# Kernel tuning notes

Measured on AMD Instinct MI355X. Metric: run time of the kernel, lower is better.

Reference implementation:

```python
import jax, jax.numpy as jnp
import numpy as np

B, S, HID = 1, 2048, 2048
NH, NKV, D = 32, 4, 128   # query heads, kv heads, head_dim
ROPE_THETA = 1e6
EPS = 1e-6


def _rms_norm(x, w):
    # per-head RMSNorm over head_dim, computed in fp32 (Qwen3MoeRMSNorm)
    xf = x.astype(jnp.float32)
    var = jnp.mean(xf * xf, axis=-1, keepdims=True)
    return (w * (xf * jax.lax.rsqrt(var + EPS))).astype(x.dtype)


def _rotate_half(x):
    x1, x2 = jnp.split(x, 2, axis=-1)
    return jnp.concatenate([-x2, x1], axis=-1)


def setup_inputs() -> dict:
    key = jax.random.key(0)
    ks = jax.random.split(key, 5)
    hidden_states = jax.random.normal(ks[0], (B, S, HID), jnp.float32)
    # weights stored as (in, out); torch Linear computes x @ W.T with W (out,in) -- same math
    wq = jax.random.normal(ks[1], (HID, NH * D), jnp.float32) * 0.02
    wk = jax.random.normal(ks[2], (HID, NKV * D), jnp.float32) * 0.02
    wv = jax.random.normal(ks[3], (HID, NKV * D), jnp.float32) * 0.02
    wo = jax.random.normal(ks[4], (NH * D, HID), jnp.float32) * 0.02
    q_norm_w = jnp.ones((D,), jnp.float32)
    k_norm_w = jnp.ones((D,), jnp.float32)
    # RoPE tables (rotate_half convention, like HF Qwen3)
    inv_freq = 1.0 / (ROPE_THETA ** (jnp.arange(0, D, 2, dtype=jnp.float32) / D))
    freqs = jnp.arange(S, dtype=jnp.float32)[:, None] * inv_freq[None, :]  # [S, D/2]
    emb = jnp.concatenate([freqs, freqs], axis=-1)  # [S, D]
    cos, sin = jnp.cos(emb), jnp.sin(emb)
    # causal mask (True = keep)
    attention_mask = jnp.tril(jnp.ones((S, S), bool))[None, None]
    return {
        'hidden_states': hidden_states, 'cos': cos, 'sin': sin,
        'wq': wq, 'wk': wk, 'wv': wv, 'wo': wo,
        'q_norm_w': q_norm_w, 'k_norm_w': k_norm_w,
        'attention_mask': attention_mask, 'start_pos': 0,
    }


def reference(hidden_states, cos, sin, wq, wk, wv, wo, q_norm_w, k_norm_w,
              attention_mask, start_pos):
    b, s, _ = hidden_states.shape
    # projections + per-head RMSNorm, then [B, H, S, D]
    q = _rms_norm((hidden_states @ wq).reshape(b, s, NH, D), q_norm_w).transpose(0, 2, 1, 3)
    k = _rms_norm((hidden_states @ wk).reshape(b, s, NKV, D), k_norm_w).transpose(0, 2, 1, 3)
    v = (hidden_states @ wv).reshape(b, s, NKV, D).transpose(0, 2, 1, 3)
    # rotary embedding (rotate_half form); start_pos=0 -> tables already aligned
    c = cos[None, None, :, :]
    sn = sin[None, None, :, :]
    q = q * c + _rotate_half(q) * sn
    k = k * c + _rotate_half(k) * sn
    # GQA: repeat kv heads to match query heads
    groups = NH // NKV
    k = jnp.repeat(k, groups, axis=1)
    v = jnp.repeat(v, groups, axis=1)
    scaling = D ** -0.5
    scores = jnp.einsum('bhqd,bhkd->bhqk', q, k) * scaling  # [B, NH, S, S]
    scores = jnp.where(attention_mask, scores, jnp.float32(-1e9))
    attn = jax.nn.softmax(scores, axis=-1)
    out = jnp.einsum('bhqk,bhkd->bhqd', attn, v)  # [B, NH, S, D]
    out = out.transpose(0, 2, 1, 3).reshape(b, s, NH * D)
    return out @ wo
```

## Files before the change

### kernel.cpp

```cpp
#include <hip/hip_runtime.h>
#include <hip/hip_bf16.h>

using short4v = __attribute__((ext_vector_type(4))) short;
using short8 = __attribute__((ext_vector_type(8))) short;
using f32x4  = __attribute__((ext_vector_type(4))) float;

#define SEQ 2048
#define NHEAD 32
#define NKVH 4
#define HDIM 128
#define QK_SCALE_LOG2 (0.08838834764831845f * 1.44269504088896340f)

__device__ __forceinline__ float fast_exp2(float x) { return __builtin_amdgcn_exp2f(x); }
__device__ __forceinline__ float b2f(short u) {
    return __uint_as_float(((unsigned)(unsigned short)u) << 16);
}
__device__ __forceinline__ short f2bb(float f) {
    __hip_bfloat16 h = __float2bfloat16(f);
    return *reinterpret_cast<short*>(&h);
}
__device__ __forceinline__ void gload_lds16(const __hip_bfloat16* src, __hip_bfloat16* dst) {
    __builtin_amdgcn_global_load_lds((const __attribute__((address_space(1))) void*)src,
                                     (__attribute__((address_space(3))) void*)dst, 16, 0, 0);
}

__global__ __launch_bounds__(256) void prep_kernel(
    const float* __restrict__ hs, __hip_bfloat16* __restrict__ hsb,
    const float* __restrict__ wq, const float* __restrict__ wk, const float* __restrict__ wv,
    const float* __restrict__ wo,
    __hip_bfloat16* __restrict__ WqkvT, __hip_bfloat16* __restrict__ WoT) {
    const int b = blockIdx.x, tid = threadIdx.x;
    if (b < 4096) {
        int i = b * 256 + tid;
        float4 v = ((const float4*)hs)[i];
        __hip_bfloat16 h4[4] = {__float2bfloat16(v.x), __float2bfloat16(v.y),
                                __float2bfloat16(v.z), __float2bfloat16(v.w)};
        ((ushort4*)hsb)[i] = *(ushort4*)h4;
        return;
    }
    __shared__ float tile[32][33];
    const float* W; __hip_bfloat16* Wt; int N, ld, nb, kb;
    if (b < 12288)      { int bb = b - 4096;  W = wq; Wt = WqkvT;                       N = 4096; ld = 2048; nb = (bb & 127) * 32; kb = (bb >> 7) * 32; }
    else if (b < 13312) { int bb = b - 12288; W = wk; Wt = WqkvT + (size_t)4096 * 2048; N = 512;  ld = 2048; nb = (bb & 15) * 32;  kb = (bb >> 4) * 32; }
    else if (b < 14336) { int bb = b - 13312; W = wv; Wt = WqkvT + (size_t)4608 * 2048; N = 512;  ld = 2048; nb = (bb & 15) * 32;  kb = (bb >> 4) * 32; }
    else                { int bb = b - 14336; W = wo; Wt = WoT;                         N = 2048; ld = 4096; nb = (bb & 63) * 32;  kb = (bb >> 6) * 32; }
    int tx = tid & 31, ty = tid >> 5;
    for (int j = 0; j < 32; j += 8)
        tile[ty + j][tx] = W[(size_t)(kb + ty + j) * N + nb + tx];
    __syncthreads();
    for (int j = 0; j < 32; j += 8)
        Wt[(size_t)(nb + ty + j) * ld + kb + tx] = __float2bfloat16(tile[tx][ty + j]);
}

__global__ void add3b_kernel(const __hip_bfloat16* __restrict__ a, const __hip_bfloat16* __restrict__ b,
                             const __hip_bfloat16* __restrict__ c, float* __restrict__ o, int n4) {
    int i = blockIdx.x * blockDim.x + threadIdx.x;
    if (i >= n4) return;
    short4v x = ((const short4v*)a)[i];
    short4v y = ((const short4v*)b)[i];
    short4v z = ((const short4v*)c)[i];
    float4 r = {b2f(x[0]) + b2f(y[0]) + b2f(z[0]), b2f(x[1]) + b2f(y[1]) + b2f(z[1]),
                b2f(x[2]) + b2f(y[2]) + b2f(z[2]), b2f(x[3]) + b2f(y[3]) + b2f(z[3])};
    ((float4*)o)[i] = r;
}

#define BM 128
#define BN 128
#define BK2 64
template <typename OutT>
__global__ __launch_bounds__(256) void gemm_bt_kernel(
    const __hip_bfloat16* __restrict__ A, const __hip_bfloat16* __restrict__ Bt,
    OutT* __restrict__ C, int M, int N, int KextMax, int ld, int koff, long long czstride, int Ktot) {
    const int kstart = blockIdx.z * koff;
    const int Kext = min(KextMax, Ktot - kstart);
    A  += (size_t)kstart;
    Bt += (size_t)kstart;
    C  += (size_t)blockIdx.z * czstride;
    __shared__ __align__(16) __hip_bfloat16 sA[BM * BK2];
    __shared__ __align__(16) __hip_bfloat16 sB[BN * BK2];
    const int tid = threadIdx.x;
    const int w = tid >> 6, l = tid & 63;
    const int wr = w >> 1, wc = w & 1;
    const int row0 = blockIdx.y * BM;
    const int col0 = blockIdx.x * BN;
    const int fr = l & 15;
    const int fq = l >> 4;
    const int xs = (fr & 7) << 4;

    f32x4 acc[4][4] = {};

    for (int k0 = 0; k0 < Kext; k0 += BK2) {
        for (int i = 0; i < 4; ++i) {
            int ch = i * 256 + tid;
            int row = ch >> 3;
            int cb = ((ch & 7) * 16) ^ ((row & 7) << 4);
            gload_lds16(A  + (size_t)(row0 + row) * ld + k0 + (cb >> 1), &sA[ch * 8]);
            gload_lds16(Bt + (size_t)(col0 + row) * ld + k0 + (cb >> 1), &sB[ch * 8]);
        }
        __syncthreads();
        short8 af[4][2], bfr[4][2];
        for (int m = 0; m < 4; ++m) {
            const char* base = (const char*)sA + (wr * 64 + m * 16 + fr) * 128;
            af[m][0] = *(const short8*)(base + (((fq) * 16)     ^ xs));
            af[m][1] = *(const short8*)(base + (((fq + 4) * 16) ^ xs));
        }
        for (int n = 0; n < 4; ++n) {
            const char* base = (const char*)sB + (wc * 64 + n * 16 + fr) * 128;
            bfr[n][0] = *(const short8*)(base + (((fq) * 16)     ^ xs));
            bfr[n][1] = *(const short8*)(base + (((fq + 4) * 16) ^ xs));
        }
        for (int kk = 0; kk < 2; ++kk)
            for (int m = 0; m < 4; ++m)
                for (int n = 0; n < 4; ++n)
                    acc[m][n] = __builtin_amdgcn_mfma_f32_16x16x32_bf16(af[m][kk], bfr[n][kk], acc[m][n], 0, 0, 0);
        __syncthreads();
    }
    for (int m = 0; m < 4; ++m)
        for (int n = 0; n < 4; ++n)
            for (int r = 0; r < 4; ++r) {
                int row = row0 + wr * 64 + m * 16 + fq * 4 + r;
                int col = col0 + wc * 64 + n * 16 + fr;
                float v = acc[m][n][r];
                if constexpr (__is_same(OutT, float)) C[(size_t)row * N + col] = v;
                else C[(size_t)row * N + col] = __float2bfloat16(v);
            }
}

__global__ __launch_bounds__(256) void pack_kernel(
    const __hip_bfloat16* __restrict__ P0, const __hip_bfloat16* __restrict__ P1,
    const float* __restrict__ cosp, const float* __restrict__ sinp,
    const float* __restrict__ qnw, const float* __restrict__ knw,
    __hip_bfloat16* __restrict__ Qh, __hip_bfloat16* __restrict__ Kh, __hip_bfloat16* __restrict__ Vt) {
    const int tid = threadIdx.x;
    const int rloc = tid >> 4, l16 = tid & 15;
    const int r = blockIdx.y * 16 + rloc;
    const int s = blockIdx.x * 2 + (r >= 40 ? 1 : 0);
    const int slot = (r >= 40) ? r - 40 : r;
    int off;
    if (slot < 32)      off = slot * 128;
    else if (slot < 36) off = 4096 + (slot - 32) * 128;
    else                off = 4608 + (slot - 36) * 128;
    const int d0 = l16 * 4;
    const size_t base = (size_t)s * 5120 + off;

    short4v a0 = *(const short4v*)&P0[base + d0];
    short4v a1 = *(const short4v*)&P0[base + d0 + 64];
    short4v b0 = *(const short4v*)&P1[base + d0];
    short4v b1 = *(const short4v*)&P1[base + d0 + 64];
    float x1[4], x2[4];
    for (int j = 0; j < 4; ++j) {
        x1[j] = b2f(a0[j]) + b2f(b0[j]);
        x2[j] = b2f(a1[j]) + b2f(b1[j]);
    }

    if (slot >= 36) {
        int t = slot - 36;
        for (int j = 0; j < 4; ++j) {
            Vt[((size_t)t * 128 + d0 + j) * SEQ + s]      = __float2bfloat16(x1[j]);
            Vt[((size_t)t * 128 + d0 + 64 + j) * SEQ + s] = __float2bfloat16(x2[j]);
        }
        return;
    }
    float ss = 0.f;
    for (int j = 0; j < 4; ++j) ss += x1[j] * x1[j] + x2[j] * x2[j];
    for (int x = 1; x < 16; x <<= 1) ss += __shfl_xor(ss, x);
    float rs = rsqrtf(ss * (1.0f / 128.0f) + 1e-6f);

    f32x4 c4 = *(const f32x4*)&cosp[(size_t)s * 128 + d0];
    f32x4 s4 = *(const f32x4*)&sinp[(size_t)s * 128 + d0];
    const float* wgt = (slot < 32) ? qnw : knw;
    f32x4 w1 = *(const f32x4*)&wgt[d0];
    f32x4 w2 = *(const f32x4*)&wgt[d0 + 64];
    const float scl = (slot < 32) ? QK_SCALE_LOG2 : 1.0f;

    short4v o1, o2;
    for (int j = 0; j < 4; ++j) {
        float a = x1[j] * rs * w1[j], b = x2[j] * rs * w2[j];
        o1[j] = f2bb((a * c4[j] - b * s4[j]) * scl);
        o2[j] = f2bb((b * c4[j] + a * s4[j]) * scl);
    }
    __hip_bfloat16* dst;
    if (slot < 32) dst = Qh + ((size_t)slot * SEQ + s) * 128;
    else           dst = Kh + ((size_t)(slot - 32) * SEQ + s) * 128;
    *(short4v*)&dst[d0]      = o1;
    *(short4v*)&dst[d0 + 64] = o2;
}

__global__ __launch_bounds__(256, 2) void attn_kernel(
    const __hip_bfloat16* __restrict__ Qh,
    const __hip_bfloat16* __restrict__ Kh,
    const __hip_bfloat16* __restrict__ Vt,
    __hip_bfloat16* __restrict__ Oa) {
    __shared__ __align__(16) __hip_bfloat16 sK[2][64 * 128];
    __shared__ __align__(16) __hip_bfloat16 sV[2][128 * 64];
    __shared__ __align__(16) __hip_bfloat16 sP[4][16 * 72];

    const int tid = threadIdx.x;
    const int w = tid >> 6, l = tid & 63;
    const int bx = blockIdx.x;
    const int y = bx & 7;
    const int qtA = bx >> 3;
    const int qbaseA = qtA * 16;
    const int qbaseB = (127 - qtA) * 16;
    const int hkv = y >> 1;
    const int h = y * 4 + w;
    const int fr = l & 15, g = l >> 4;

    const __hip_bfloat16* Kp = Kh + (size_t)hkv * SEQ * HDIM;
    const __hip_bfloat16* Vp = Vt + (size_t)hkv * HDIM * SEQ;
    char* myP = (char*)&sP[w][0];

    short8 qfA[4], qfB[4];
    {
        const __hip_bfloat16* QpA = Qh + ((size_t)h * SEQ + qbaseA) * HDIM;
        const __hip_bfloat16* QpB = Qh + ((size_t)h * SEQ + qbaseB) * HDIM;
        for (int c = 0; c < 4; ++c) {
            qfA[c] = *(const short8*)&QpA[fr * HDIM + c * 32 + g * 8];
            qfB[c] = *(const short8*)&QpB[fr * HDIM + c * 32 + g * 8];
        }
    }

    f32x4 oaccA[8] = {}, oaccB[8] = {};
    float msA = -3.0e38f, lsA = 0.f;
    float msB = -3.0e38f, lsB = 0.f;

    const int xr = (fr & 7) << 4;
    const int qgA = qbaseA + fr;
    const int qgB = qbaseB + fr;
    const int nA = ((qbaseA + 15) >> 6) + 1;
    const int nB = ((qbaseB + 15) >> 6) + 1;

    auto stage = [&](int buf, int kbase) {
        for (int i = 0; i < 4; ++i) {
            int blk = i * 4 + w;
            {
                int row = blk * 4 + (l >> 4);
                int cb = ((l & 15) * 16) ^ ((row & 7) << 4);
                gload_lds16(Kp + (size_t)(kbase + row) * HDIM + (cb >> 1), &sK[buf][blk * 512]);
            }
            {
                int row = blk * 8 + (l >> 3);
                int cb = ((l & 7) * 16) ^ ((row & 7) << 4);
                gload_lds16(Vp + (size_t)row * SEQ + kbase + (cb >> 1), &sV[buf][blk * 512]);
            }
        }
    };

#define PROCESS(QF, OACC, MS, LS, QG, QBASE)                                           \
    {                                                                                  \
        f32x4 s[4] = {};                                                               \
        __builtin_amdgcn_s_setprio(1);                                                 \
        for (int j = 0; j < 4; ++j) {                                                  \
            const __hip_bfloat16* kp = &sK[buf][(j * 16 + fr) * 128];                  \
            for (int c = 0; c < 4; ++c) {                                              \
                short8 kf = *(const short8*)&kp[((c * 64 + g * 16) ^ xr) >> 1];        \
                s[j] = __builtin_amdgcn_mfma_f32_16x16x32_bf16(kf, QF[c], s[j], 0, 0, 0); \
            }                                                                          \
        }                                                                              \
        __builtin_amdgcn_s_setprio(0);                                                 \
        float v[4][4];                                                                 \
        const bool full = (kbase + 63 <= (QBASE));                                     \
        if (full) {                                                                    \
            for (int j = 0; j < 4; ++j)                                                \
                for (int r = 0; r < 4; ++r) v[j][r] = s[j][r];                         \
        } else {                                                                       \
            const int kb0 = kbase + g * 4;                                             \
            for (int j = 0; j < 4; ++j)                                                \
                for (int r = 0; r < 4; ++r)                                            \
                    v[j][r] = (kb0 + j * 16 + r <= (QG)) ? s[j][r] : -1e30f;           \
        }                                                                              \
        float m0 = fmaxf(fmaxf(v[0][0], v[0][1]), fmaxf(v[0][2], v[0][3]));            \
        float m1 = fmaxf(fmaxf(v[1][0], v[1][1]), fmaxf(v[1][2], v[1][3]));            \
        float m2 = fmaxf(fmaxf(v[2][0], v[2][1]), fmaxf(v[2][2], v[2][3]));            \
        float m3 = fmaxf(fmaxf(v[3][0], v[3][1]), fmaxf(v[3][2], v[3][3]));            \
        float m = fmaxf(fmaxf(m0, m1), fmaxf(m2, m3));                                 \
        m = fmaxf(m, __shfl_xor(m, 16));                                               \
        m = fmaxf(m, __shfl_xor(m, 32));                                               \
        if (__any(m > MS + 12.0f)) {                                                   \
            float mnew = fmaxf(MS, m);                                                 \
            float corr = fast_exp2(MS - mnew);                                         \
            MS = mnew;                                                                 \
            LS *= corr;                                                                \
            float c0 = __shfl(corr, g * 4 + 0);                                        \
            float c1 = __shfl(corr, g * 4 + 1);                                        \
            float c2 = __shfl(corr, g * 4 + 2);                                        \
            float c3 = __shfl(corr, g * 4 + 3);                                        \
            for (int dt = 0; dt < 8; ++dt) {                                           \
                OACC[dt][0] *= c0; OACC[dt][1] *= c1;                                  \
                OACC[dt][2] *= c2; OACC[dt][3] *= c3;                                  \
            }                                                                          \
        }                                                                              \
        for (int j = 0; j < 4; ++j) {                                                  \
            float e0 = fast_exp2(v[j][0] - MS);                                        \
            float e1 = fast_exp2(v[j][1] - MS);                                        \
            float e2 = fast_exp2(v[j][2] - MS);                                        \
            float e3 = fast_exp2(v[j][3] - MS);                                        \
            LS += (e0 + e1) + (e2 + e3);                                               \
            short4v pw = {f2bb(e0), f2bb(e1), f2bb(e2), f2bb(e3)};                     \
            *(short4v*)(myP + fr * 144 + j * 32 + g * 8) = pw;                         \
        }                                                                              \
        short8 pa0 = *(const short8*)(myP + fr * 144 + g * 16);                        \
        short8 pa1 = *(const short8*)(myP + fr * 144 + 64 + g * 16);                   \
        __builtin_amdgcn_s_setprio(1);                                                 \
        for (int dt = 0; dt < 8; ++dt) {                                               \
            const __hip_bfloat16* vp = &sV[buf][(dt * 16 + fr) * 64];                  \
            short8 vb0 = *(const short8*)&vp[((g * 16)      ^ xr) >> 1];               \
            short8 vb1 = *(const short8*)&vp[((g * 16 + 64) ^ xr) >> 1];               \
            OACC[dt] = __builtin_amdgcn_mfma_f32_16x16x32_bf16(pa0, vb0, OACC[dt], 0, 0, 0); \
            OACC[dt] = __builtin_amdgcn_mfma_f32_16x16x32_bf16(pa1, vb1, OACC[dt], 0, 0, 0); \
        }                                                                              \
        __builtin_amdgcn_s_setprio(0);                                                 \
    }

    stage(0, 0);
    __syncthreads();

    for (int t = 0; t < nB; ++t) {
        const int kbase = t * 64;
        const int buf = t & 1;
        if (t + 1 < nB) stage(buf ^ 1, kbase + 64);

        if (t < nA) PROCESS(qfA, oaccA, msA, lsA, qgA, qbaseA);
        PROCESS(qfB, oaccB, msB, lsB, qgB, qbaseB);

        __syncthreads();
    }
#undef PROCESS

    lsA += __shfl_xor(lsA, 16); lsA += __shfl_xor(lsA, 32);
    lsB += __shfl_xor(lsB, 16); lsB += __shfl_xor(lsB, 32);
    float invA[4], invB[4];
    for (int r = 0; r < 4; ++r) {
        invA[r] = 1.0f / __shfl(lsA, g * 4 + r);
        invB[r] = 1.0f / __shfl(lsB, g * 4 + r);
    }
    for (int dt = 0; dt < 8; ++dt)
        for (int r = 0; r < 4; ++r) {
            int qA = qbaseA + g * 4 + r;
            int qB = qbaseB + g * 4 + r;
            Oa[(size_t)qA * (NHEAD * HDIM) + h * HDIM + dt * 16 + fr] =
                __float2bfloat16(oaccA[dt][r] * invA[r]);
            Oa[(size_t)qB * (NHEAD * HDIM) + h * HDIM + dt * 16 + fr] =
                __float2bfloat16(oaccB[dt][r] * invB[r]);
        }
}

extern "C" void kernel_launch(void* const* d_in, const int* in_sizes, int n_in,
                              void* d_out, int out_size, void* d_ws, size_t ws_size,
                              hipStream_t stream) {
    const float* hs   = (const float*)d_in[0];
    const float* cosp = (const float*)d_in[1];
    const float* sinp = (const float*)d_in[2];
    const float* wq   = (const float*)d_in[3];
    const float* wk   = (const float*)d_in[4];
    const float* wv   = (const float*)d_in[5];
    const float* wo   = (const float*)d_in[6];
    const float* qnw  = (const float*)d_in[7];
    const float* knw  = (const float*)d_in[8];
    float* out = (float*)d_out;
    char* ws = (char*)d_ws;

    __hip_bfloat16* hsb    = (__hip_bfloat16*)(ws);
    __hip_bfloat16* WqkvT  = (__hip_bfloat16*)(ws + 8388608);
    __hip_bfloat16* WoT    = (__hip_bfloat16*)(ws + 29360128);
    __hip_bfloat16* P0     = (__hip_bfloat16*)(ws + 46137344);
    __hip_bfloat16* P1     = (__hip_bfloat16*)(ws + 67108864);
    __hip_bfloat16* Qh     = (__hip_bfloat16*)(ws + 8388608);
    __hip_bfloat16* Kh     = (__hip_bfloat16*)(ws + 25165824);
    __hip_bfloat16* Vt     = (__hip_bfloat16*)(ws + 27262976);
    __hip_bfloat16* Oa     = (__hip_bfloat16*)(ws + 46137344);
    __hip_bfloat16* Qb     = (__hip_bfloat16*)(ws);

    prep_kernel<<<22528, 256, 0, stream>>>(hs, hsb, wq, wk, wv, wo, WqkvT, WoT);
    gemm_bt_kernel<__hip_bfloat16><<<dim3(40, 16, 2), 256, 0, stream>>>(
        hsb, WqkvT, P0, 2048, 5120, 1024, 2048, 1024, 10485760LL, 2048);
    pack_kernel<<<dim3(1024, 5), 256, 0, stream>>>(P0, P1, cosp, sinp, qnw, knw, Qh, Kh, Vt);
    attn_kernel<<<dim3(512), 256, 0, stream>>>(Qh, Kh, Vt, Oa);
    gemm_bt_kernel<__hip_bfloat16><<<dim3(16, 16, 3), 256, 0, stream>>>(
        Oa, WoT, Qb, 2048, 2048, 1408, 4096, 1408, 4194304LL, 4096);
    add3b_kernel<<<4096, 256, 0, stream>>>(Qb, Qb + 4194304, Qb + 8388608, out, (2048 * 2048) / 4);
}
```

Before: 209.2 us.

## Fuse QKV projection with RMSNorm, RoPE and V transpose in one GEMM

Replaces the split-K QKV GEMM (two partial outputs) plus a separate pack kernel with a single full-K GEMM. Its epilogue stages each 128x128 head tile in LDS, applies per-head RMSNorm, RoPE and Q scaling, and writes Q, K and transposed V directly. This removes the partial-sum round trip through global memory and one kernel launch. The cost is fewer blocks (640 instead of 1280) with a longer K loop, so parallelism and load latency hiding drop, and the workspace layout is reshuffled.

```diff
diff --git a/kernel.cpp b/kernel.cpp
--- a/kernel.cpp
+++ b/kernel.cpp
@@ -126,64 +126,105 @@
             }
 }
 
-__global__ __launch_bounds__(256) void pack_kernel(
-    const __hip_bfloat16* __restrict__ P0, const __hip_bfloat16* __restrict__ P1,
+__global__ __launch_bounds__(256) void gemm_qkv2_kernel(
+    const __hip_bfloat16* __restrict__ A,
+    const __hip_bfloat16* __restrict__ Bt,
     const float* __restrict__ cosp, const float* __restrict__ sinp,
     const float* __restrict__ qnw, const float* __restrict__ knw,
-    __hip_bfloat16* __restrict__ Qh, __hip_bfloat16* __restrict__ Kh, __hip_bfloat16* __restrict__ Vt) {
+    __hip_bfloat16* __restrict__ Qh, __hip_bfloat16* __restrict__ Kh,
+    __hip_bfloat16* __restrict__ Vt) {
+    __shared__ __align__(16) char pool[128 * 132 * 2];
+    __hip_bfloat16* sA     = (__hip_bfloat16*)pool;
+    __hip_bfloat16* sB     = (__hip_bfloat16*)(pool + 16384);
+    __hip_bfloat16* stageT = (__hip_bfloat16*)pool;
+
     const int tid = threadIdx.x;
-    const int rloc = tid >> 4, l16 = tid & 15;
-    const int r = blockIdx.y * 16 + rloc;
-    const int s = blockIdx.x * 2 + (r >= 40 ? 1 : 0);
-    const int slot = (r >= 40) ? r - 40 : r;
-    int off;
-    if (slot < 32)      off = slot * 128;
-    else if (slot < 36) off = 4096 + (slot - 32) * 128;
-    else                off = 4608 + (slot - 36) * 128;
-    const int d0 = l16 * 4;
-    const size_t base = (size_t)s * 5120 + off;
-
-    short4v a0 = *(const short4v*)&P0[base + d0];
-    short4v a1 = *(const short4v*)&P0[base + d0 + 64];
-    short4v b0 = *(const short4v*)&P1[base + d0];
-    short4v b1 = *(const short4v*)&P1[base + d0 + 64];
-    float x1[4], x2[4];
-    for (int j = 0; j < 4; ++j) {
-        x1[j] = b2f(a0[j]) + b2f(b0[j]);
-        x2[j] = b2f(a1[j]) + b2f(b1[j]);
-    }
-
-    if (slot >= 36) {
-        int t = slot - 36;
-        for (int j = 0; j < 4; ++j) {
-            Vt[((size_t)t * 128 + d0 + j) * SEQ + s]      = __float2bfloat16(x1[j]);
-            Vt[((size_t)t * 128 + d0 + 64 + j) * SEQ + s] = __float2bfloat16(x2[j]);
-        }
-        return;
-    }
-    float ss = 0.f;
-    for (int j = 0; j < 4; ++j) ss += x1[j] * x1[j] + x2[j] * x2[j];
-    for (int x = 1; x < 16; x <<= 1) ss += __shfl_xor(ss, x);
-    float rs = rsqrtf(ss * (1.0f / 128.0f) + 1e-6f);
-
-    f32x4 c4 = *(const f32x4*)&cosp[(size_t)s * 128 + d0];
-    f32x4 s4 = *(const f32x4*)&sinp[(size_t)s * 128 + d0];
-    const float* wgt = (slot < 32) ? qnw : knw;
-    f32x4 w1 = *(const f32x4*)&wgt[d0];
-    f32x4 w2 = *(const f32x4*)&wgt[d0 + 64];
-    const float scl = (slot < 32) ? QK_SCALE_LOG2 : 1.0f;
-
-    short4v o1, o2;
-    for (int j = 0; j < 4; ++j) {
-        float a = x1[j] * rs * w1[j], b = x2[j] * rs * w2[j];
-        o1[j] = f2bb((a * c4[j] - b * s4[j]) * scl);
-        o2[j] = f2bb((b * c4[j] + a * s4[j]) * scl);
-    }
-    __hip_bfloat16* dst;
-    if (slot < 32) dst = Qh + ((size_t)slot * SEQ + s) * 128;
-    else           dst = Kh + ((size_t)(slot - 32) * SEQ + s) * 128;
-    *(short4v*)&dst[d0]      = o1;
-    *(short4v*)&dst[d0 + 64] = o2;
+    const int w = tid >> 6, l = tid & 63;
+    const int wr = w >> 1, wc = w & 1;
+    const int slot = blockIdx.x;
+    const int row0 = blockIdx.y * BM;
+    const int col0 = slot * BN;
+    const int fr = l & 15;
+    const int fq = l >> 4;
+    const int xs = (fr & 7) << 4;
+
+    f32x4 acc[4][4] = {};
+
+    for (int k0 = 0; k0 < 2048; k0 += BK2) {
+        for (int i = 0; i < 4; ++i) {
+            int ch = i * 256 + tid;
+            int row = ch >> 3;
+            int cb = ((ch & 7) * 16) ^ ((row & 7) << 4);
+            gload_lds16(A  + (size_t)(row0 + row) * 2048 + k0 + (cb >> 1), &sA[ch * 8]);
+            gload_lds16(Bt + (size_t)(col0 + row) * 2048 + k0 + (cb >> 1), &sB[ch * 8]);
+        }
+        __syncthreads();
+        short8 af[4][2], bfr[4][2];
+        for (int m = 0; m < 4; ++m) {
+            const char* base = (const char*)sA + (wr * 64 + m * 16 + fr) * 128;
+            af[m][0] = *(const short8*)(base + (((fq) * 16)     ^ xs));
+            af[m][1] = *(const short8*)(base + (((fq + 4) * 16) ^ xs));
+        }
+        for (int n = 0; n < 4; ++n) {
+            const char* base = (const char*)sB + (wc * 64 + n * 16 + fr) * 128;
+            bfr[n][0] = *(const short8*)(base + (((fq) * 16)     ^ xs));
+            bfr[n][1] = *(const short8*)(base + (((fq + 4) * 16) ^ xs));
+        }
+        for (int kk = 0; kk < 2; ++kk)
+            for (int m = 0; m < 4; ++m)
+                for (int n = 0; n < 4; ++n)
+                    acc[m][n] = __builtin_amdgcn_mfma_f32_16x16x32_bf16(af[m][kk], bfr[n][kk], acc[m][n], 0, 0, 0);
+        __syncthreads();
+    }
+
+    for (int m = 0; m < 4; ++m)
+        for (int n = 0; n < 4; ++n) {
+            short4v pw = {f2bb(acc[m][n][0]), f2bb(acc[m][n][1]),
+                          f2bb(acc[m][n][2]), f2bb(acc[m][n][3])};
+            *(short4v*)&stageT[(wc * 64 + n * 16 + fr) * 132 + wr * 64 + m * 16 + fq * 4] = pw;
+        }
+    __syncthreads();
+
+    if (slot < 36) {
+        const float* wgt = (slot < 32) ? qnw : knw;
+        const float scl = (slot < 32) ? QK_SCALE_LOG2 : 1.0f;
+        const int rloc = tid >> 4, l16 = tid & 15;
+        const int d0 = l16 * 4;
+        f32x4 w1 = *(const f32x4*)&wgt[d0];
+        f32x4 w2 = *(const f32x4*)&wgt[d0 + 64];
+        for (int pass = 0; pass < 8; ++pass) {
+            const int row = pass * 16 + rloc;
+            const int s = row0 + row;
+            float x1[4], x2[4];
+            for (int jj = 0; jj < 4; ++jj) {
+                x1[jj] = b2f(*(const short*)&stageT[(d0 + jj) * 132 + row]);
+                x2[jj] = b2f(*(const short*)&stageT[(d0 + 64 + jj) * 132 + row]);
+            }
+            float ssq = 0.f;
+            for (int jj = 0; jj < 4; ++jj) ssq += x1[jj] * x1[jj] + x2[jj] * x2[jj];
+            for (int x = 1; x < 16; x <<= 1) ssq += __shfl_xor(ssq, x);
+            float rs = rsqrtf(ssq * (1.0f / 128.0f) + 1e-6f);
+            f32x4 c4 = *(const f32x4*)&cosp[(size_t)s * 128 + d0];
+            f32x4 s4 = *(const f32x4*)&sinp[(size_t)s * 128 + d0];
+            short4v o1, o2;
+            for (int jj = 0; jj < 4; ++jj) {
+                float a = x1[jj] * rs * w1[jj], b = x2[jj] * rs * w2[jj];
+                o1[jj] = f2bb((a * c4[jj] - b * s4[jj]) * scl);
+                o2[jj] = f2bb((b * c4[jj] + a * s4[jj]) * scl);
+            }
+            __hip_bfloat16* dst = (slot < 32)
+                ? Qh + ((size_t)slot * SEQ + s) * 128
+                : Kh + ((size_t)(slot - 32) * SEQ + s) * 128;
+            *(short4v*)&dst[d0]      = o1;
+            *(short4v*)&dst[d0 + 64] = o2;
+        }
+    } else {
+        const int d = tid >> 1, sh = tid & 1;
+        __hip_bfloat16* dst = Vt + ((size_t)(slot - 36) * 128 + d) * SEQ + row0 + sh * 64;
+        const __hip_bfloat16* src = &stageT[d * 132 + sh * 64];
+        for (int j = 0; j < 16; ++j)
+            *(short4v*)&dst[j * 4] = *(const short4v*)&src[j * 4];
+    }
 }
 
 __global__ __launch_bounds__(256, 2) void attn_kernel(
@@ -363,18 +404,15 @@
     __hip_bfloat16* hsb    = (__hip_bfloat16*)(ws);
     __hip_bfloat16* WqkvT  = (__hip_bfloat16*)(ws + 8388608);
     __hip_bfloat16* WoT    = (__hip_bfloat16*)(ws + 29360128);
-    __hip_bfloat16* P0     = (__hip_bfloat16*)(ws + 46137344);
-    __hip_bfloat16* P1     = (__hip_bfloat16*)(ws + 67108864);
-    __hip_bfloat16* Qh     = (__hip_bfloat16*)(ws + 8388608);
-    __hip_bfloat16* Kh     = (__hip_bfloat16*)(ws + 25165824);
-    __hip_bfloat16* Vt     = (__hip_bfloat16*)(ws + 27262976);
-    __hip_bfloat16* Oa     = (__hip_bfloat16*)(ws + 46137344);
-    __hip_bfloat16* Qb     = (__hip_bfloat16*)(ws);
+    __hip_bfloat16* Qh     = (__hip_bfloat16*)(ws + 46137344);
+    __hip_bfloat16* Kh     = (__hip_bfloat16*)(ws + 62914560);
+    __hip_bfloat16* Vt     = (__hip_bfloat16*)(ws + 65011712);
+    __hip_bfloat16* Oa     = (__hip_bfloat16*)(ws + 8388608);
+    __hip_bfloat16* Qb     = (__hip_bfloat16*)(ws + 46137344);
 
     prep_kernel<<<22528, 256, 0, stream>>>(hs, hsb, wq, wk, wv, wo, WqkvT, WoT);
-    gemm_bt_kernel<__hip_bfloat16><<<dim3(40, 16, 2), 256, 0, stream>>>(
-        hsb, WqkvT, P0, 2048, 5120, 1024, 2048, 1024, 10485760LL, 2048);
-    pack_kernel<<<dim3(1024, 5), 256, 0, stream>>>(P0, P1, cosp, sinp, qnw, knw, Qh, Kh, Vt);
+    gemm_qkv2_kernel<<<dim3(40, 16), 256, 0, stream>>>(
+        hsb, WqkvT, cosp, sinp, qnw, knw, Qh, Kh, Vt);
     attn_kernel<<<dim3(512), 256, 0, stream>>>(Qh, Kh, Vt, Oa);
     gemm_bt_kernel<__hip_bfloat16><<<dim3(16, 16, 3), 256, 0, stream>>>(
         Oa, WoT, Qb, 2048, 2048, 1408, 4096, 1408, 4194304LL, 4096);
```

Result: slower. 217.0 us (+3.7%).
